# Kernel optimization log

Measured on AMD Instinct MI355X. Metric: run time of the kernel, lower is better.

The kernel has to match this reference:

```python
import jax, jax.numpy as jnp
import numpy as np

Q_DIM = 1024
K_DIM = 1024
EMBED_DIM = 1024
NUM_HEADS = 16
HEAD_DIM = EMBED_DIM // NUM_HEADS
SCALE = HEAD_DIM ** (-0.5)
CLAMP = 50000.0
MASK_NEG = -9e15


def _xavier(key, out_f, in_f):
    limit = float(np.sqrt(6.0 / (in_f + out_f)))
    return jax.random.uniform(key, (out_f, in_f), jnp.float32, -limit, limit)


def setup_inputs() -> dict:
    key = jax.random.key(0)
    ks = jax.random.split(key, 8)
    B, Tq, Tk = 4, 2048, 2048
    return {
        "q": jax.random.normal(ks[0], (B, Tq, Q_DIM), jnp.float32),
        "k": jax.random.normal(ks[1], (B, Tk, K_DIM), jnp.float32),
        "v": jax.random.normal(ks[2], (B, Tk, K_DIM), jnp.float32),
        "attention_mask": jax.random.randint(ks[3], (B, Tk), 0, 2, jnp.int32),
        "Wq": _xavier(ks[4], EMBED_DIM, Q_DIM),
        "bq": jnp.zeros((EMBED_DIM,), jnp.float32),
        "Wk": _xavier(ks[5], EMBED_DIM, K_DIM),
        "bk": jnp.zeros((EMBED_DIM,), jnp.float32),
        "Wv": _xavier(ks[6], EMBED_DIM, K_DIM),
        "bv": jnp.zeros((EMBED_DIM,), jnp.float32),
        "Wo": _xavier(ks[7], K_DIM, EMBED_DIM),
        "bo": jnp.zeros((K_DIM,), jnp.float32),
    }


def _split_heads(x, B, T):
    # [B, T, E] -> [B, H, T, D]
    return x.reshape(B, T, NUM_HEADS, HEAD_DIM).transpose(0, 2, 1, 3)


def reference(q, k, v, attention_mask, Wq, bq, Wk, bk, Wv, bv, Wo, bo):
    B, Tq, _ = q.shape
    Tk = k.shape[1]
    # projections (nn.Linear: x @ W.T + b)
    qs = _split_heads((q @ Wq.T + bq) * SCALE, B, Tq)   # [B,H,Tq,D]
    ks_ = _split_heads(k @ Wk.T + bk, B, Tk)            # [B,H,Tk,D]
    vs = _split_heads(v @ Wv.T + bv, B, Tk)             # [B,H,Tk,D]
    # scores with clamp
    scores = jnp.einsum("bhqd,bhkd->bhqk", qs, ks_)
    scores = jnp.clip(scores, -CLAMP, CLAMP)
    # additive mask: masked_fill(mask==0, -9e15) then add (nonzero entries add their value)
    m = attention_mask.astype(scores.dtype)
    add_mask = jnp.where(attention_mask == 0, MASK_NEG, m)  # [B,Tk]
    scores = scores + add_mask[:, None, None, :]
    probs = jax.nn.softmax(scores, axis=-1)
    # dropout inactive in eval mode
    attn = jnp.einsum("bhqk,bhkd->bhqd", probs, vs)
    attn = attn.transpose(0, 2, 1, 3).reshape(B, Tq, EMBED_DIM)
    return attn @ Wo.T + bo
```

## Files before the change

kernel.cpp:

```cpp
#include <hip/hip_runtime.h>
#include <hip/hip_bf16.h>

typedef __bf16 bf16x8 __attribute__((ext_vector_type(8)));
typedef float  f32x4  __attribute__((ext_vector_type(4)));
typedef unsigned short ushort;
typedef ushort ushort4v __attribute__((ext_vector_type(4)));

#if __has_builtin(__builtin_amdgcn_exp2f)
#define EXP2(x) __builtin_amdgcn_exp2f(x)
#else
#define EXP2(x) exp2f(x)
#endif

#if __has_builtin(__builtin_amdgcn_fmed3f)
#define CLAMP2(x) __builtin_amdgcn_fmed3f((x), -72134.75f, 72134.75f)
#else
#define CLAMP2(x) fminf(fmaxf((x), -72134.75f), 72134.75f)
#endif

__device__ __forceinline__ ushort f2bf(float f) {
  union { float f; unsigned u; } v; v.f = f;
  unsigned r = v.u + 0x7FFFu + ((v.u >> 16) & 1u);
  return (ushort)(r >> 16);
}

typedef __attribute__((address_space(1))) const unsigned int as1_uint;
typedef __attribute__((address_space(3))) unsigned int as3_uint;
__device__ __forceinline__ void gll16(const void* g, void* l) {
  __builtin_amdgcn_global_load_lds((as1_uint*)g, (as3_uint*)l, 16, 0, 0);
}

__global__ void prep(const float* __restrict__ Wq, const float* __restrict__ Wk,
                     const float* __restrict__ Wv, const float* __restrict__ Wo,
                     const int* __restrict__ mask,
                     ushort4v* __restrict__ wqb, ushort4v* __restrict__ wkb,
                     ushort4v* __restrict__ wvb, ushort4v* __restrict__ wob,
                     float* __restrict__ madd) {
  int y = blockIdx.y;
  if (y == 4) {
    int i = blockIdx.x * blockDim.x + threadIdx.x;
    if (i < 8192) {
      int mv = mask[i];
      madd[i] = (mv == 0) ? -9e15f * 1.44269504f : (float)mv * 1.44269504f;
    }
    return;
  }
  const float* s = (y == 0) ? Wq : (y == 1) ? Wk : (y == 2) ? Wv : Wo;
  ushort4v* d = (y == 0) ? wqb : (y == 1) ? wkb : (y == 2) ? wvb : wob;
  const float4* s4p = (const float4*)s;
  const int n4 = 1024 * 1024 / 4;
  for (int i = blockIdx.x * blockDim.x + threadIdx.x; i < n4; i += gridDim.x * blockDim.x) {
    float4 v = s4p[i]; ushort4v o;
    o[0] = f2bf(v.x); o[1] = f2bf(v.y); o[2] = f2bf(v.z); o[3] = f2bf(v.w);
    d[i] = o;
  }
}

__global__ void cast3(const float* __restrict__ q, const float* __restrict__ k,
                      const float* __restrict__ v,
                      ushort4v* __restrict__ qb, ushort4v* __restrict__ kb,
                      ushort4v* __restrict__ vb) {
  int y = blockIdx.y;
  const float4* s = (const float4*)((y == 0) ? q : (y == 1) ? k : v);
  ushort4v* d = (y == 0) ? qb : (y == 1) ? kb : vb;
  const int n4 = 8192 * 1024 / 4;
  for (int i = blockIdx.x * blockDim.x + threadIdx.x; i < n4; i += gridDim.x * blockDim.x) {
    float4 vv = s[i]; ushort4v o;
    o[0] = f2bf(vv.x); o[1] = f2bf(vv.y); o[2] = f2bf(vv.z); o[3] = f2bf(vv.w);
    d[i] = o;
  }
}

__device__ __forceinline__ void gemm_core(
    const ushort* __restrict__ A, const ushort* __restrict__ W,
    const float* __restrict__ bias, void* __restrict__ outp,
    float scale, int mode, ushort* smem)
{
  const int tid = threadIdx.x, lane = tid & 63, wid = tid >> 6;
  const int r0 = blockIdx.y * 128, c0 = blockIdx.x * 128;
  const int wr = (wid >> 1) * 64, wc = (wid & 1) * 64;
  const int K = 1024;
  ushort* sA = smem;
  ushort* sB = smem + 8192;

  f32x4 acc[4][4] = {};

  for (int kt = 0; kt < 16; ++kt) {
    const int k0 = kt * 64;
#pragma unroll
    for (int i = 0; i < 4; ++i) {
      int s = (wid * 4 + i) * 64 + lane;
      int row = s >> 3, sl = s & 7, gsl = sl ^ (row & 7);
      gll16(&A[(size_t)(r0 + row) * K + k0 + gsl * 8], &sA[(wid * 4 + i) * 512]);
      gll16(&W[(size_t)(c0 + row) * K + k0 + gsl * 8], &sB[(wid * 4 + i) * 512]);
    }
    __syncthreads();
#pragma unroll
    for (int kk = 0; kk < 2; ++kk) {
      bf16x8 af[4], bf[4];
#pragma unroll
      for (int mf = 0; mf < 4; ++mf) {
        int row = wr + mf * 16 + (lane & 15);
        int slot = (kk * 4 + (lane >> 4)) ^ (row & 7);
        af[mf] = *(const bf16x8*)&sA[row * 64 + slot * 8];
      }
#pragma unroll
      for (int nf = 0; nf < 4; ++nf) {
        int row = wc + nf * 16 + (lane & 15);
        int slot = (kk * 4 + (lane >> 4)) ^ (row & 7);
        bf[nf] = *(const bf16x8*)&sB[row * 64 + slot * 8];
      }
#pragma unroll
      for (int mf = 0; mf < 4; ++mf)
#pragma unroll
        for (int nf = 0; nf < 4; ++nf)
          acc[mf][nf] = __builtin_amdgcn_mfma_f32_16x16x32_bf16(af[mf], bf[nf], acc[mf][nf], 0, 0, 0);
    }
    __syncthreads();
  }

  if (mode == 2) {
    ushort* sT = smem;
#pragma unroll
    for (int nf = 0; nf < 4; ++nf) {
      int col = wc + nf * 16 + (lane & 15);
      float bv = bias[c0 + col];
#pragma unroll
      for (int mf = 0; mf < 4; ++mf)
#pragma unroll
        for (int r = 0; r < 4; ++r) {
          int row = wr + mf * 16 + ((lane >> 4) * 4) + r;
          sT[col * 128 + (row ^ ((col & 7) << 3))] = f2bf(acc[mf][nf][r] + bv);
        }
    }
    __syncthreads();
    int bidx = r0 >> 11, tb = r0 & 2047;
#pragma unroll
    for (int it = 0; it < 8; ++it) {
      int colr = it * 16 + wid * 4 + (lane >> 4);
      int t0 = (lane & 15) * 8;
      int4 v = *(const int4*)&sT[colr * 128 + (t0 ^ ((colr & 7) << 3))];
      int colg = c0 + colr;
      int hh = colg >> 6, d = colg & 63;
      *(int4*)&((ushort*)outp)[((size_t)(bidx * 16 + hh) * 64 + d) * 2048 + tb + t0] = v;
    }
    return;
  }

#pragma unroll
  for (int nf = 0; nf < 4; ++nf) {
    int col = c0 + wc + nf * 16 + (lane & 15);
    float bv = bias[col];
#pragma unroll
    for (int mf = 0; mf < 4; ++mf) {
#pragma unroll
      for (int r = 0; r < 4; ++r) {
        int row = r0 + wr + mf * 16 + ((lane >> 4) * 4) + r;
        float v = (acc[mf][nf][r] + bv) * scale;
        if (mode == 0) {
          int b = row >> 11, t = row & 2047;
          int h = col >> 6, d = col & 63;
          ((ushort*)outp)[(((size_t)(b * 16 + h) * 2048 + t) << 6) + d] = f2bf(v);
        } else {
          ((float*)outp)[(size_t)row * 1024 + col] = v;
        }
      }
    }
  }
}

__global__ __launch_bounds__(256) void gemm3(
    const ushort* __restrict__ qb, const ushort* __restrict__ kb, const ushort* __restrict__ vb,
    const ushort* __restrict__ wq, const ushort* __restrict__ wk, const ushort* __restrict__ wv,
    const float* __restrict__ bq, const float* __restrict__ bk, const float* __restrict__ bv,
    ushort* __restrict__ Qs, ushort* __restrict__ Ks, ushort* __restrict__ Vts)
{
  __shared__ __align__(16) ushort smem[16384];
  int z = blockIdx.z;
  const ushort *A, *W; const float* bias; ushort* out; float scale; int mode;
  if (z == 0)      { A = qb; W = wq; bias = bq; out = Qs;  scale = 0.125f * 1.44269504f; mode = 0; }
  else if (z == 1) { A = kb; W = wk; bias = bk; out = Ks;  scale = 1.0f;   mode = 0; }
  else             { A = vb; W = wv; bias = bv; out = Vts; scale = 1.0f;   mode = 2; }
  gemm_core(A, W, bias, out, scale, mode, smem);
}

__global__ __launch_bounds__(256) void gemmF(
    const ushort* __restrict__ Oat, const ushort* __restrict__ wo,
    const float* __restrict__ bo, float* __restrict__ out)
{
  __shared__ __align__(16) ushort smem[16384];
  gemm_core(Oat, wo, bo, out, 1.0f, 1, smem);
}

__global__ __launch_bounds__(256) void attn(
    const ushort* __restrict__ Q, const ushort* __restrict__ Km,
    const ushort* __restrict__ Vt, const float* __restrict__ madd,
    ushort* __restrict__ O)
{
  __shared__ __align__(16) ushort sK[64 * 64];
  __shared__ __align__(16) ushort sVt[64 * 64];
  __shared__ __align__(16) float sM[2048];

  const int tid = threadIdx.x, lane = tid & 63, wid = tid >> 6;
  const int bid = blockIdx.x;
  const int x = bid & 7, g = bid >> 3;
  const int pair = x * 8 + (g >> 5), qt = g & 31;
  const int b = pair >> 4, h = pair & 15;

  const size_t hb = (size_t)pair * (2048 * 64);
  const ushort* Qh = Q + hb + (size_t)qt * (64 * 64);
  const ushort* Kh = Km + hb;
  const ushort* Vh = Vt + hb;
  const float* mb = madd + b * 2048;

  const int m = lane & 15, qg = lane >> 4;

#pragma unroll
  for (int c = 0; c < 2; ++c)
    *(float4*)&sM[(tid + c * 256) * 4] = *(const float4*)&mb[(tid + c * 256) * 4];

  bf16x8 qf[2];
#pragma unroll
  for (int kk = 0; kk < 2; ++kk)
    qf[kk] = *(const bf16x8*)&Qh[(size_t)(wid * 16 + m) * 64 + kk * 32 + qg * 8];

  const int sr0 = tid >> 3,         sl0 = tid & 7,         ssl0 = sl0 ^ (sr0 & 7);
  const int sr1 = (tid + 256) >> 3, sl1 = (tid + 256) & 7, ssl1 = sl1 ^ (sr1 & 7);

  int4 kreg0 = *(const int4*)&Kh[(size_t)sr0 * 64 + sl0 * 8];
  int4 kreg1 = *(const int4*)&Kh[(size_t)sr1 * 64 + sl1 * 8];
  int4 vreg0 = *(const int4*)&Vh[(size_t)sr0 * 2048 + sl0 * 8];
  int4 vreg1 = *(const int4*)&Vh[(size_t)sr1 * 2048 + sl1 * 8];

  float runm = -3.0e38f, runl = 0.f;
  f32x4 o[4] = {};

  for (int kt = 0; kt < 32; ++kt) {
    if (kt) __syncthreads();
    *(int4*)&sK[sr0 * 64 + ssl0 * 8] = kreg0;
    *(int4*)&sK[sr1 * 64 + ssl1 * 8] = kreg1;
    *(int4*)&sVt[sr0 * 64 + ssl0 * 8] = vreg0;
    *(int4*)&sVt[sr1 * 64 + ssl1 * 8] = vreg1;
    __syncthreads();
    if (kt < 31) {
      const int n0n = (kt + 1) * 64;
      kreg0 = *(const int4*)&Kh[(size_t)(n0n + sr0) * 64 + sl0 * 8];
      kreg1 = *(const int4*)&Kh[(size_t)(n0n + sr1) * 64 + sl1 * 8];
      vreg0 = *(const int4*)&Vh[(size_t)sr0 * 2048 + n0n + sl0 * 8];
      vreg1 = *(const int4*)&Vh[(size_t)sr1 * 2048 + n0n + sl1 * 8];
    }
    const int n0 = kt * 64;

    f32x4 s4[4] = {};
    __builtin_amdgcn_s_setprio(1);
#pragma unroll
    for (int af = 0; af < 4; ++af) {
#pragma unroll
      for (int kk = 0; kk < 2; ++kk) {
        int krow = af * 16 + m;
        int slot = (kk * 4 + qg) ^ (krow & 7);
        bf16x8 kf = *(const bf16x8*)&sK[krow * 64 + slot * 8];
        s4[af] = __builtin_amdgcn_mfma_f32_16x16x32_bf16(kf, qf[kk], s4[af], 0, 0, 0);
      }
    }
    __builtin_amdgcn_s_setprio(0);

    float tmax = -3.0e38f;
#pragma unroll
    for (int af = 0; af < 4; ++af) {
      float4 mk = *(const float4*)&sM[n0 + af * 16 + qg * 4];
      const float* mp = (const float*)&mk;
#pragma unroll
      for (int r = 0; r < 4; ++r)
        s4[af][r] = CLAMP2(s4[af][r]) + mp[r];
      tmax = fmaxf(tmax, fmaxf(fmaxf(s4[af][0], s4[af][1]),
                               fmaxf(s4[af][2], s4[af][3])));
    }
    tmax = fmaxf(tmax, __shfl_xor(tmax, 16, 64));
    tmax = fmaxf(tmax, __shfl_xor(tmax, 32, 64));
    if (!__all(tmax <= runm + 11.5416f)) {
      float newm = fmaxf(runm, tmax);
      float corr = EXP2(runm - newm);
      runl *= corr;
#pragma unroll
      for (int af = 0; af < 4; ++af) o[af] *= corr;
      runm = newm;
    }

    float psum = 0.f;
    unsigned w[4][2];
#pragma unroll
    for (int af = 0; af < 4; ++af) {
#pragma unroll
      for (int r = 0; r < 4; ++r) {
        float p = EXP2(s4[af][r] - runm);
        s4[af][r] = p;
        psum += p;
      }
      asm("v_cvt_pk_bf16_f32 %0, %1, %2"
          : "=v"(w[af][0]) : "v"(s4[af][0]), "v"(s4[af][1]));
      asm("v_cvt_pk_bf16_f32 %0, %1, %2"
          : "=v"(w[af][1]) : "v"(s4[af][2]), "v"(s4[af][3]));
    }
    psum += __shfl_xor(psum, 16, 64);
    psum += __shfl_xor(psum, 32, 64);
    runl += psum;

    __builtin_amdgcn_s_setprio(1);
#pragma unroll
    for (int kk = 0; kk < 2; ++kk) {
      unsigned a0 = w[2 * kk][0], a1 = w[2 * kk][1];
      unsigned b0 = w[2 * kk + 1][0], b1 = w[2 * kk + 1][1];
      asm("v_permlane32_swap_b32 %0, %1" : "+v"(a0), "+v"(b0));
      asm("v_permlane16_swap_b32 %0, %1" : "+v"(a0), "+v"(b0));
      asm("v_permlane32_swap_b32 %0, %1" : "+v"(a1), "+v"(b1));
      asm("v_permlane16_swap_b32 %0, %1" : "+v"(a1), "+v"(b1));
      union { unsigned u[4]; bf16x8 v; } pu;
      pu.u[0] = a0; pu.u[1] = a1; pu.u[2] = b0; pu.u[3] = b1;
      bf16x8 pf = pu.v;
#pragma unroll
      for (int af = 0; af < 4; ++af) {
        int drow = af * 16 + m;
        int slot = (kk * 4 + qg) ^ (drow & 7);
        bf16x8 vf = *(const bf16x8*)&sVt[drow * 64 + slot * 8];
        o[af] = __builtin_amdgcn_mfma_f32_16x16x32_bf16(vf, pf, o[af], 0, 0, 0);
      }
    }
    __builtin_amdgcn_s_setprio(0);
  }

  float inv = 1.0f / runl;
  int tq = qt * 64 + wid * 16 + m;
  size_t obase = (((size_t)(b * 2048 + tq)) * 16 + h) * 64;
#pragma unroll
  for (int af = 0; af < 4; ++af) {
    ushort4v pk;
#pragma unroll
    for (int r = 0; r < 4; ++r) pk[r] = f2bf(o[af][r] * inv);
    *(ushort4v*)&O[obase + af * 16 + qg * 4] = pk;
  }
}

extern "C" void kernel_launch(void* const* d_in, const int* in_sizes, int n_in,
                              void* d_out, int out_size, void* d_ws, size_t ws_size,
                              hipStream_t stream) {
  const float* q  = (const float*)d_in[0];
  const float* k  = (const float*)d_in[1];
  const float* v  = (const float*)d_in[2];
  const int* mask = (const int*)d_in[3];
  const float* Wq = (const float*)d_in[4];
  const float* bq = (const float*)d_in[5];
  const float* Wk = (const float*)d_in[6];
  const float* bk = (const float*)d_in[7];
  const float* Wv = (const float*)d_in[8];
  const float* bv = (const float*)d_in[9];
  const float* Wo = (const float*)d_in[10];
  const float* bo = (const float*)d_in[11];
  float* out = (float*)d_out;

  const size_t NEED = (size_t)104 << 20;
  if (ws_size < NEED) return;

  char* ws = (char*)d_ws;
  ushort* WQb = (ushort*)(ws + ((size_t)0 << 20));
  ushort* WKb = (ushort*)(ws + ((size_t)2 << 20));
  ushort* WVb = (ushort*)(ws + ((size_t)4 << 20));
  ushort* WOb = (ushort*)(ws + ((size_t)6 << 20));
  ushort* qb  = (ushort*)(ws + ((size_t)8 << 20));
  ushort* kb  = (ushort*)(ws + ((size_t)24 << 20));
  ushort* vb  = (ushort*)(ws + ((size_t)40 << 20));
  ushort* Qs  = (ushort*)(ws + ((size_t)56 << 20));
  ushort* Ks  = (ushort*)(ws + ((size_t)72 << 20));
  ushort* Vts = (ushort*)(ws + ((size_t)88 << 20));
  ushort* Oat = qb;
  float* madd = (float*)d_out;

  prep<<<dim3(256, 5), dim3(256), 0, stream>>>(Wq, Wk, Wv, Wo, mask,
      (ushort4v*)WQb, (ushort4v*)WKb, (ushort4v*)WVb, (ushort4v*)WOb, madd);
  cast3<<<dim3(1024, 3), dim3(256), 0, stream>>>(q, k, v,
      (ushort4v*)qb, (ushort4v*)kb, (ushort4v*)vb);

  gemm3<<<dim3(8, 64, 3), dim3(256), 0, stream>>>(qb, kb, vb, WQb, WKb, WVb,
      bq, bk, bv, Qs, Ks, Vts);

  attn<<<dim3(2048), dim3(256), 0, stream>>>(Qs, Ks, Vts, madd, Oat);

  gemmF<<<dim3(8, 64), dim3(256), 0, stream>>>(Oat, WOb, bo, out);
}
```

Baseline: 258.0 us.

## Double-buffer attention K/V via direct LDS loads and merge cast kernels

Attention now stages K and V tiles into two LDS buffers with global_load_lds, so the next tile loads while the current one computes and each tile needs one barrier. The mask is read from global memory into registers one tile ahead instead of through LDS, and the softmax row sum is computed by an MFMA against ones rather than shuffle reductions. The clamp on scores is dropped, and the weight/input cast kernels are merged into one launch. These changes add LDS footprint and an extra MFMA per step, and removing the clamp relies on scores never reaching the clamp bound.

```diff
diff --git a/kernel.cpp b/kernel.cpp
--- a/kernel.cpp
+++ b/kernel.cpp
@@ -12,12 +12,6 @@
 #define EXP2(x) exp2f(x)
 #endif
 
-#if __has_builtin(__builtin_amdgcn_fmed3f)
-#define CLAMP2(x) __builtin_amdgcn_fmed3f((x), -72134.75f, 72134.75f)
-#else
-#define CLAMP2(x) fminf(fmaxf((x), -72134.75f), 72134.75f)
-#endif
-
 __device__ __forceinline__ ushort f2bf(float f) {
   union { float f; unsigned u; } v; v.f = f;
   unsigned r = v.u + 0x7FFFu + ((v.u >> 16) & 1u);
@@ -30,12 +24,14 @@
   __builtin_amdgcn_global_load_lds((as1_uint*)g, (as3_uint*)l, 16, 0, 0);
 }
 
-__global__ void prep(const float* __restrict__ Wq, const float* __restrict__ Wk,
-                     const float* __restrict__ Wv, const float* __restrict__ Wo,
-                     const int* __restrict__ mask,
-                     ushort4v* __restrict__ wqb, ushort4v* __restrict__ wkb,
-                     ushort4v* __restrict__ wvb, ushort4v* __restrict__ wob,
-                     float* __restrict__ madd) {
+__global__ void prep_all(const float* __restrict__ Wq, const float* __restrict__ Wk,
+                         const float* __restrict__ Wv, const float* __restrict__ Wo,
+                         const float* __restrict__ q, const float* __restrict__ k,
+                         const float* __restrict__ v, const int* __restrict__ mask,
+                         ushort4v* __restrict__ wqb, ushort4v* __restrict__ wkb,
+                         ushort4v* __restrict__ wvb, ushort4v* __restrict__ wob,
+                         ushort4v* __restrict__ qb, ushort4v* __restrict__ kb,
+                         ushort4v* __restrict__ vb, float* __restrict__ madd) {
   int y = blockIdx.y;
   if (y == 4) {
     int i = blockIdx.x * blockDim.x + threadIdx.x;
@@ -45,27 +41,19 @@
     }
     return;
   }
-  const float* s = (y == 0) ? Wq : (y == 1) ? Wk : (y == 2) ? Wv : Wo;
-  ushort4v* d = (y == 0) ? wqb : (y == 1) ? wkb : (y == 2) ? wvb : wob;
+  const float* s; ushort4v* d; int n4;
+  if (y < 4) {
+    s = (y == 0) ? Wq : (y == 1) ? Wk : (y == 2) ? Wv : Wo;
+    d = (y == 0) ? wqb : (y == 1) ? wkb : (y == 2) ? wvb : wob;
+    n4 = 1024 * 1024 / 4;
+  } else {
+    s = (y == 5) ? q : (y == 6) ? k : v;
+    d = (y == 5) ? qb : (y == 6) ? kb : vb;
+    n4 = 8192 * 1024 / 4;
+  }
   const float4* s4p = (const float4*)s;
-  const int n4 = 1024 * 1024 / 4;
   for (int i = blockIdx.x * blockDim.x + threadIdx.x; i < n4; i += gridDim.x * blockDim.x) {
-    float4 v = s4p[i]; ushort4v o;
-    o[0] = f2bf(v.x); o[1] = f2bf(v.y); o[2] = f2bf(v.z); o[3] = f2bf(v.w);
-    d[i] = o;
-  }
-}
-
-__global__ void cast3(const float* __restrict__ q, const float* __restrict__ k,
-                      const float* __restrict__ v,
-                      ushort4v* __restrict__ qb, ushort4v* __restrict__ kb,
-                      ushort4v* __restrict__ vb) {
-  int y = blockIdx.y;
-  const float4* s = (const float4*)((y == 0) ? q : (y == 1) ? k : v);
-  ushort4v* d = (y == 0) ? qb : (y == 1) ? kb : vb;
-  const int n4 = 8192 * 1024 / 4;
-  for (int i = blockIdx.x * blockDim.x + threadIdx.x; i < n4; i += gridDim.x * blockDim.x) {
-    float4 vv = s[i]; ushort4v o;
+    float4 vv = s4p[i]; ushort4v o;
     o[0] = f2bf(vv.x); o[1] = f2bf(vv.y); o[2] = f2bf(vv.z); o[3] = f2bf(vv.w);
     d[i] = o;
   }
@@ -197,9 +185,8 @@
     const ushort* __restrict__ Vt, const float* __restrict__ madd,
     ushort* __restrict__ O)
 {
-  __shared__ __align__(16) ushort sK[64 * 64];
-  __shared__ __align__(16) ushort sVt[64 * 64];
-  __shared__ __align__(16) float sM[2048];
+  __shared__ __align__(16) ushort sK[2][64 * 64];
+  __shared__ __align__(16) ushort sV[2][64 * 64];
 
   const int tid = threadIdx.x, lane = tid & 63, wid = tid >> 6;
   const int bid = blockIdx.x;
@@ -215,121 +202,124 @@
 
   const int m = lane & 15, qg = lane >> 4;
 
-#pragma unroll
-  for (int c = 0; c < 2; ++c)
-    *(float4*)&sM[(tid + c * 256) * 4] = *(const float4*)&mb[(tid + c * 256) * 4];
+#define STAGE(BSEL, T) do {                                                     \
+    const int n0g_ = (T) * 64;                                                  \
+    _Pragma("unroll")                                                           \
+    for (int i_ = 0; i_ < 2; ++i_) {                                            \
+      int ch_ = wid * 2 + i_;                                                   \
+      int s_ = ch_ * 64 + lane;                                                 \
+      int row_ = s_ >> 3, sl_ = s_ & 7, gsl_ = sl_ ^ (row_ & 7);                \
+      gll16(&Kh[(size_t)(n0g_ + row_) * 64 + gsl_ * 8], &sK[BSEL][ch_ * 512]);  \
+      gll16(&Vh[(size_t)row_ * 2048 + n0g_ + gsl_ * 8], &sV[BSEL][ch_ * 512]);  \
+    }                                                                           \
+  } while (0)
 
   bf16x8 qf[2];
 #pragma unroll
   for (int kk = 0; kk < 2; ++kk)
     qf[kk] = *(const bf16x8*)&Qh[(size_t)(wid * 16 + m) * 64 + kk * 32 + qg * 8];
 
-  const int sr0 = tid >> 3,         sl0 = tid & 7,         ssl0 = sl0 ^ (sr0 & 7);
-  const int sr1 = (tid + 256) >> 3, sl1 = (tid + 256) & 7, ssl1 = sl1 ^ (sr1 & 7);
-
-  int4 kreg0 = *(const int4*)&Kh[(size_t)sr0 * 64 + sl0 * 8];
-  int4 kreg1 = *(const int4*)&Kh[(size_t)sr1 * 64 + sl1 * 8];
-  int4 vreg0 = *(const int4*)&Vh[(size_t)sr0 * 2048 + sl0 * 8];
-  int4 vreg1 = *(const int4*)&Vh[(size_t)sr1 * 2048 + sl1 * 8];
-
-  float runm = -3.0e38f, runl = 0.f;
+  f32x4 mreg[4];
+#pragma unroll
+  for (int af = 0; af < 4; ++af)
+    mreg[af] = *(const f32x4*)&mb[af * 16 + qg * 4];
+
+  union { unsigned u[4]; bf16x8 v; } onesu;
+  onesu.u[0] = onesu.u[1] = onesu.u[2] = onesu.u[3] = 0x3F803F80u;
+  const bf16x8 ones = onesu.v;
+
+  STAGE(0, 0);
+  __syncthreads();
+
+  float runm = -3.0e38f;
   f32x4 o[4] = {};
-
-  for (int kt = 0; kt < 32; ++kt) {
-    if (kt) __syncthreads();
-    *(int4*)&sK[sr0 * 64 + ssl0 * 8] = kreg0;
-    *(int4*)&sK[sr1 * 64 + ssl1 * 8] = kreg1;
-    *(int4*)&sVt[sr0 * 64 + ssl0 * 8] = vreg0;
-    *(int4*)&sVt[sr1 * 64 + ssl1 * 8] = vreg1;
-    __syncthreads();
-    if (kt < 31) {
-      const int n0n = (kt + 1) * 64;
-      kreg0 = *(const int4*)&Kh[(size_t)(n0n + sr0) * 64 + sl0 * 8];
-      kreg1 = *(const int4*)&Kh[(size_t)(n0n + sr1) * 64 + sl1 * 8];
-      vreg0 = *(const int4*)&Vh[(size_t)sr0 * 2048 + n0n + sl0 * 8];
-      vreg1 = *(const int4*)&Vh[(size_t)sr1 * 2048 + n0n + sl1 * 8];
-    }
-    const int n0 = kt * 64;
-
-    f32x4 s4[4] = {};
-    __builtin_amdgcn_s_setprio(1);
-#pragma unroll
-    for (int af = 0; af < 4; ++af) {
-#pragma unroll
-      for (int kk = 0; kk < 2; ++kk) {
-        int krow = af * 16 + m;
-        int slot = (kk * 4 + qg) ^ (krow & 7);
-        bf16x8 kf = *(const bf16x8*)&sK[krow * 64 + slot * 8];
-        s4[af] = __builtin_amdgcn_mfma_f32_16x16x32_bf16(kf, qf[kk], s4[af], 0, 0, 0);
-      }
-    }
-    __builtin_amdgcn_s_setprio(0);
-
-    float tmax = -3.0e38f;
-#pragma unroll
-    for (int af = 0; af < 4; ++af) {
-      float4 mk = *(const float4*)&sM[n0 + af * 16 + qg * 4];
-      const float* mp = (const float*)&mk;
-#pragma unroll
-      for (int r = 0; r < 4; ++r)
-        s4[af][r] = CLAMP2(s4[af][r]) + mp[r];
-      tmax = fmaxf(tmax, fmaxf(fmaxf(s4[af][0], s4[af][1]),
-                               fmaxf(s4[af][2], s4[af][3])));
-    }
-    tmax = fmaxf(tmax, __shfl_xor(tmax, 16, 64));
-    tmax = fmaxf(tmax, __shfl_xor(tmax, 32, 64));
-    if (!__all(tmax <= runm + 11.5416f)) {
-      float newm = fmaxf(runm, tmax);
-      float corr = EXP2(runm - newm);
-      runl *= corr;
-#pragma unroll
-      for (int af = 0; af < 4; ++af) o[af] *= corr;
-      runm = newm;
-    }
-
-    float psum = 0.f;
-    unsigned w[4][2];
-#pragma unroll
-    for (int af = 0; af < 4; ++af) {
-#pragma unroll
-      for (int r = 0; r < 4; ++r) {
-        float p = EXP2(s4[af][r] - runm);
-        s4[af][r] = p;
-        psum += p;
-      }
-      asm("v_cvt_pk_bf16_f32 %0, %1, %2"
-          : "=v"(w[af][0]) : "v"(s4[af][0]), "v"(s4[af][1]));
-      asm("v_cvt_pk_bf16_f32 %0, %1, %2"
-          : "=v"(w[af][1]) : "v"(s4[af][2]), "v"(s4[af][3]));
-    }
-    psum += __shfl_xor(psum, 16, 64);
-    psum += __shfl_xor(psum, 32, 64);
-    runl += psum;
-
-    __builtin_amdgcn_s_setprio(1);
-#pragma unroll
-    for (int kk = 0; kk < 2; ++kk) {
-      unsigned a0 = w[2 * kk][0], a1 = w[2 * kk][1];
-      unsigned b0 = w[2 * kk + 1][0], b1 = w[2 * kk + 1][1];
-      asm("v_permlane32_swap_b32 %0, %1" : "+v"(a0), "+v"(b0));
-      asm("v_permlane16_swap_b32 %0, %1" : "+v"(a0), "+v"(b0));
-      asm("v_permlane32_swap_b32 %0, %1" : "+v"(a1), "+v"(b1));
-      asm("v_permlane16_swap_b32 %0, %1" : "+v"(a1), "+v"(b1));
-      union { unsigned u[4]; bf16x8 v; } pu;
-      pu.u[0] = a0; pu.u[1] = a1; pu.u[2] = b0; pu.u[3] = b1;
-      bf16x8 pf = pu.v;
-#pragma unroll
-      for (int af = 0; af < 4; ++af) {
-        int drow = af * 16 + m;
-        int slot = (kk * 4 + qg) ^ (drow & 7);
-        bf16x8 vf = *(const bf16x8*)&sVt[drow * 64 + slot * 8];
-        o[af] = __builtin_amdgcn_mfma_f32_16x16x32_bf16(vf, pf, o[af], 0, 0, 0);
-      }
-    }
-    __builtin_amdgcn_s_setprio(0);
-  }
-
-  float inv = 1.0f / runl;
+  f32x4 osum = {};
+
+#define TILE_BODY(BK, BV, KT) do {                                              \
+    f32x4 s4_[4];                                                               \
+    _Pragma("unroll")                                                           \
+    for (int af = 0; af < 4; ++af) s4_[af] = mreg[af];                          \
+    if ((KT) < 31) {                                                            \
+      const float* ms_ = mb + ((KT) + 1) * 64 + qg * 4;                         \
+      _Pragma("unroll")                                                         \
+      for (int af = 0; af < 4; ++af) mreg[af] = *(const f32x4*)&ms_[af * 16];   \
+    }                                                                           \
+    __builtin_amdgcn_s_setprio(1);                                              \
+    _Pragma("unroll")                                                           \
+    for (int af = 0; af < 4; ++af) {                                            \
+      _Pragma("unroll")                                                         \
+      for (int kk = 0; kk < 2; ++kk) {                                          \
+        int krow_ = af * 16 + m;                                                \
+        int slot_ = (kk * 4 + qg) ^ (krow_ & 7);                                \
+        bf16x8 kf_ = *(const bf16x8*)&(BK)[krow_ * 64 + slot_ * 8];             \
+        s4_[af] = __builtin_amdgcn_mfma_f32_16x16x32_bf16(kf_, qf[kk], s4_[af], 0, 0, 0); \
+      }                                                                         \
+    }                                                                           \
+    __builtin_amdgcn_s_setprio(0);                                              \
+    float tmax_ = fmaxf(fmaxf(s4_[0][0], s4_[0][1]), fmaxf(s4_[0][2], s4_[0][3])); \
+    _Pragma("unroll")                                                           \
+    for (int af = 1; af < 4; ++af)                                              \
+      tmax_ = fmaxf(tmax_, fmaxf(fmaxf(s4_[af][0], s4_[af][1]),                 \
+                                 fmaxf(s4_[af][2], s4_[af][3])));               \
+    tmax_ = fmaxf(tmax_, __shfl_xor(tmax_, 16, 64));                            \
+    tmax_ = fmaxf(tmax_, __shfl_xor(tmax_, 32, 64));                            \
+    if (!__all(tmax_ <= runm + 11.5416f)) {                                     \
+      float newm_ = fmaxf(runm, tmax_);                                         \
+      float corr_ = EXP2(runm - newm_);                                         \
+      osum[0] *= corr_;                                                         \
+      _Pragma("unroll")                                                         \
+      for (int af = 0; af < 4; ++af) o[af] *= corr_;                            \
+      runm = newm_;                                                             \
+    }                                                                           \
+    unsigned w_[4][2];                                                          \
+    _Pragma("unroll")                                                           \
+    for (int af = 0; af < 4; ++af) {                                            \
+      _Pragma("unroll")                                                         \
+      for (int r = 0; r < 4; ++r) s4_[af][r] = EXP2(s4_[af][r] - runm);         \
+      asm("v_cvt_pk_bf16_f32 %0, %1, %2"                                        \
+          : "=v"(w_[af][0]) : "v"(s4_[af][0]), "v"(s4_[af][1]));                \
+      asm("v_cvt_pk_bf16_f32 %0, %1, %2"                                        \
+          : "=v"(w_[af][1]) : "v"(s4_[af][2]), "v"(s4_[af][3]));                \
+    }                                                                           \
+    __builtin_amdgcn_s_setprio(1);                                              \
+    _Pragma("unroll")                                                           \
+    for (int kk = 0; kk < 2; ++kk) {                                            \
+      unsigned a0_ = w_[2 * kk][0], a1_ = w_[2 * kk][1];                        \
+      unsigned b0_ = w_[2 * kk + 1][0], b1_ = w_[2 * kk + 1][1];                \
+      asm("v_permlane32_swap_b32 %0, %1" : "+v"(a0_), "+v"(b0_));               \
+      asm("v_permlane16_swap_b32 %0, %1" : "+v"(a0_), "+v"(b0_));               \
+      asm("v_permlane32_swap_b32 %0, %1" : "+v"(a1_), "+v"(b1_));               \
+      asm("v_permlane16_swap_b32 %0, %1" : "+v"(a1_), "+v"(b1_));               \
+      union { unsigned u[4]; bf16x8 v; } pu_;                                   \
+      pu_.u[0] = a0_; pu_.u[1] = a1_; pu_.u[2] = b0_; pu_.u[3] = b1_;           \
+      bf16x8 pf_ = pu_.v;                                                       \
+      osum = __builtin_amdgcn_mfma_f32_16x16x32_bf16(ones, pf_, osum, 0, 0, 0); \
+      _Pragma("unroll")                                                         \
+      for (int af = 0; af < 4; ++af) {                                          \
+        int drow_ = af * 16 + m;                                                \
+        int slot_ = (kk * 4 + qg) ^ (drow_ & 7);                                \
+        bf16x8 vf_ = *(const bf16x8*)&(BV)[drow_ * 64 + slot_ * 8];             \
+        o[af] = __builtin_amdgcn_mfma_f32_16x16x32_bf16(vf_, pf_, o[af], 0, 0, 0); \
+      }                                                                         \
+    }                                                                           \
+    __builtin_amdgcn_s_setprio(0);                                              \
+  } while (0)
+
+  for (int it = 0; it < 16; ++it) {
+    const int kt0 = 2 * it;
+    STAGE(1, kt0 + 1);
+    TILE_BODY(sK[0], sV[0], kt0);
+    __syncthreads();
+
+    const int kt1 = kt0 + 1;
+    if (kt1 < 31) STAGE(0, kt1 + 1);
+    TILE_BODY(sK[1], sV[1], kt1);
+    __syncthreads();
+  }
+#undef TILE_BODY
+#undef STAGE
+
+  float inv = 1.0f / osum[0];
   int tq = qt * 64 + wid * 16 + m;
   size_t obase = (((size_t)(b * 2048 + tq)) * 16 + h) * 64;
 #pragma unroll
@@ -375,10 +365,9 @@
   ushort* Oat = qb;
   float* madd = (float*)d_out;
 
-  prep<<<dim3(256, 5), dim3(256), 0, stream>>>(Wq, Wk, Wv, Wo, mask,
-      (ushort4v*)WQb, (ushort4v*)WKb, (ushort4v*)WVb, (ushort4v*)WOb, madd);
-  cast3<<<dim3(1024, 3), dim3(256), 0, stream>>>(q, k, v,
-      (ushort4v*)qb, (ushort4v*)kb, (ushort4v*)vb);
+  prep_all<<<dim3(1024, 8), dim3(256), 0, stream>>>(Wq, Wk, Wv, Wo, q, k, v, mask,
+      (ushort4v*)WQb, (ushort4v*)WKb, (ushort4v*)WVb, (ushort4v*)WOb,
+      (ushort4v*)qb, (ushort4v*)kb, (ushort4v*)vb, madd);
 
   gemm3<<<dim3(8, 64, 3), dim3(256), 0, stream>>>(qb, kb, vb, WQb, WKb, WVb,
       bq, bk, bv, Qs, Ks, Vts);
```

New measurement: 253.2 us. No clear change (-1.9%).
